# Kernel tuning notes

Hardware: AMD Instinct MI355X
Metric: run time of the kernel (lower is better)

## Reference

```python
import jax, jax.numpy as jnp
import numpy as np

B, L, DIM, H = 2, 2048, 1024, 16
HD = DIM // H  # head dim = 64
MASK_SCALE = -10 * 6  # faithful to the original source: mask_expand *= -10 * 6


def setup_inputs() -> dict:
    key = jax.random.key(0)
    ks = jax.random.split(key, 8)
    s = 1.0 / np.sqrt(DIM)
    return {
        "x": jax.random.normal(ks[0], (B, L, DIM), jnp.float32),
        "attention_mask": jax.random.uniform(ks[1], (B, L, L), jnp.float32),
        "Wq": jax.random.normal(ks[2], (DIM, DIM), jnp.float32) * s,
        "bq": jnp.zeros((DIM,), jnp.float32),
        "Wk": jax.random.normal(ks[3], (DIM, DIM), jnp.float32) * s,
        "bk": jnp.zeros((DIM,), jnp.float32),
        "Wv": jax.random.normal(ks[4], (DIM, DIM), jnp.float32) * s,
        "bv": jnp.zeros((DIM,), jnp.float32),
    }


def _split_heads(t):
    # [B, L, DIM] -> [B, H, L, HD]
    return t.reshape(B, L, H, HD).transpose(0, 2, 1, 3)


def reference(x, attention_mask, Wq, bq, Wk, bk, Wv, bv):
    q = _split_heads(x @ Wq + bq)
    k = _split_heads(x @ Wk + bk)
    v = _split_heads(x @ Wv + bv)
    scale = float(HD) ** -0.5
    # full [B, H, L, L] score matrix, as in the original
    scores = jnp.einsum("bhqd,bhkd->bhqk", q, k) * scale
    scores = scores + attention_mask[:, None, :, :] * MASK_SCALE
    probs = jax.nn.softmax(scores, axis=-1)
    ctx = jnp.einsum("bhqk,bhkd->bhqd", probs, v)
    # merge heads back: [B, L, DIM]
    return ctx.transpose(0, 2, 1, 3).reshape(B, L, DIM)
```

## Files before the change

kernel.cpp:

```cpp
#include <hip/hip_runtime.h>

#define LL 2048
#define NHEADS 16
#define HDIM 64
#define QSCALE 0.18033688011112042f
#define MASKC1 -86.56170245333780f

typedef __attribute__((ext_vector_type(8))) __bf16 bf16x8;
typedef __attribute__((ext_vector_type(4))) float f32x4;
typedef __attribute__((ext_vector_type(4))) unsigned int u32x4;

__device__ __forceinline__ unsigned short f2bf(float f) {
  unsigned int u = __builtin_bit_cast(unsigned int, f);
  u += 0x7fffu + ((u >> 16) & 1u);
  return (unsigned short)(u >> 16);
}

__device__ __forceinline__ bf16x8 ld_frag(const unsigned short* p) {
  return *reinterpret_cast<const bf16x8*>(p);
}

__device__ __forceinline__ float bflo(unsigned int u) {
  return __builtin_bit_cast(float, u << 16);
}
__device__ __forceinline__ float bfhi(unsigned int u) {
  return __builtin_bit_cast(float, u & 0xffff0000u);
}
__device__ __forceinline__ unsigned int pack2(float hi, float lo) {
  return __builtin_amdgcn_perm(__builtin_bit_cast(unsigned int, hi),
                               __builtin_bit_cast(unsigned int, lo), 0x07060302u);
}

__device__ __forceinline__ void async_cp16(const unsigned short* g, unsigned short* l) {
  __builtin_amdgcn_global_load_lds(
      (const __attribute__((address_space(1))) unsigned int*)(unsigned long long)(g),
      (__attribute__((address_space(3))) unsigned int*)(unsigned int)(unsigned long long)(l),
      16, 0, 0);
}

__global__ __launch_bounds__(256) void cvt_x_kernel(const float* __restrict__ x,
                                                    unsigned short* __restrict__ xb) {
  int i = (blockIdx.x * 256 + threadIdx.x) * 4;
  float4 v = *reinterpret_cast<const float4*>(x + i);
  ushort4 o;
  o.x = f2bf(v.x); o.y = f2bf(v.y); o.z = f2bf(v.z); o.w = f2bf(v.w);
  *reinterpret_cast<ushort4*>(xb + i) = o;
}

__global__ __launch_bounds__(256) void transpose_w_kernel(const float* __restrict__ Wq,
                                                          const float* __restrict__ Wk,
                                                          const float* __restrict__ Wv,
                                                          unsigned short* __restrict__ WtAll) {
  int z = blockIdx.z;
  const float* W = (z == 0) ? Wq : (z == 1) ? Wk : Wv;
  unsigned short* dst = WtAll + (size_t)z * 1024 * 1024;
  int n0 = blockIdx.x * 64, k0 = blockIdx.y * 64;
  __shared__ float t[64][65];
  int tx = threadIdx.x & 63, ty = threadIdx.x >> 6;
#pragma unroll
  for (int p = 0; p < 16; ++p) {
    int kr = p * 4 + ty;
    t[kr][tx] = W[(size_t)(k0 + kr) * 1024 + n0 + tx];
  }
  __syncthreads();
#pragma unroll
  for (int p = 0; p < 16; ++p) {
    int nr = p * 4 + ty;
    dst[(size_t)(n0 + nr) * 1024 + k0 + tx] = f2bf(t[tx][nr]);
  }
}

__global__ __launch_bounds__(256) void lem_prep_kernel(const float* __restrict__ mask,
                                                       unsigned short* __restrict__ lem) {
  const int qb = blockIdx.x, kt = blockIdx.y, b = blockIdx.z;
  const int tid = threadIdx.x;
  __shared__ unsigned short lds[128 * 72];
  {
    const int r0 = tid >> 4;
    const int c0 = (tid & 15) * 4;
#pragma unroll
    for (int p = 0; p < 8; ++p) {
      int row = p * 16 + r0;
      float4 v = *reinterpret_cast<const float4*>(
          mask + ((size_t)b * LL + qb * 128 + row) * LL + kt * 64 + c0);
      ushort4 o;
      o.x = f2bf(v.x * MASKC1); o.y = f2bf(v.y * MASKC1);
      o.z = f2bf(v.z * MASKC1); o.w = f2bf(v.w * MASKC1);
      *reinterpret_cast<ushort4*>(&lds[row * 72 + c0]) = o;
    }
  }
  __syncthreads();
  const int w = tid >> 6, lane = tid & 63, g = lane >> 4, cc = lane & 15;
  unsigned int ow[16];
#pragma unroll
  for (int mt = 0; mt < 2; ++mt) {
    const int q = w * 32 + mt * 16 + cc;
#pragma unroll
    for (int nt = 0; nt < 4; ++nt) {
      uint2 v = *reinterpret_cast<const uint2*>(&lds[q * 72 + nt * 16 + g * 4]);
      ow[mt * 8 + nt * 2]     = v.x;
      ow[mt * 8 + nt * 2 + 1] = v.y;
    }
  }
  uint4* dst = reinterpret_cast<uint4*>(
      lem + ((((size_t)b * 16 + qb) * 32 + kt) * 256 + tid) * 32);
#pragma unroll
  for (int j = 0; j < 4; ++j)
    dst[j] = make_uint4(ow[4 * j], ow[4 * j + 1], ow[4 * j + 2], ow[4 * j + 3]);
}

__global__ __launch_bounds__(256) void qkv_gemm_kernel(
    const unsigned short* __restrict__ xb, const unsigned short* __restrict__ WtAll,
    const float* __restrict__ bq, const float* __restrict__ bk, const float* __restrict__ bv,
    unsigned short* __restrict__ qkv) {
  const int z = blockIdx.z;
  const unsigned short* Wt = WtAll + (size_t)z * 1024 * 1024;
  const float* bias = (z == 0) ? bq : (z == 1) ? bk : bv;
  unsigned short* outb = qkv + (size_t)z * 4194304;

  __shared__ __align__(16) unsigned short smem[16384];
  unsigned short* As = smem;
  unsigned short* Bs = smem + 8192;

  const int tid = threadIdx.x;
  const int w = tid >> 6, lane = tid & 63, g = lane >> 4, cc = lane & 15;
  const int wm = w >> 1, wn = w & 1;
  const int m0 = blockIdx.y * 128, n0 = blockIdx.x * 128;
  const int srow = lane >> 3;
  const int gc = ((lane & 7) - srow) & 7;
  const unsigned short* ga = xb + (size_t)(m0 + w * 32 + srow) * 1024 + gc * 8;
  const unsigned short* gb = Wt + (size_t)(n0 + w * 32 + srow) * 1024 + gc * 8;
  unsigned short* la = As + w * 2048;
  unsigned short* lb = Bs + w * 2048;

  f32x4 acc[4][4];
#pragma unroll
  for (int i = 0; i < 4; ++i)
#pragma unroll
    for (int j = 0; j < 4; ++j) acc[i][j] = (f32x4)0.0f;

  for (int kk = 0; kk < 1024; kk += 64) {
    __syncthreads();
#pragma unroll
    for (int i = 0; i < 4; ++i) {
      async_cp16(ga + i * 8192 + kk, la + i * 512);
      async_cp16(gb + i * 8192 + kk, lb + i * 512);
    }
    __syncthreads();
    bf16x8 af[4][2], bfr[4][2];
#pragma unroll
    for (int mt = 0; mt < 4; ++mt)
#pragma unroll
      for (int ks = 0; ks < 2; ++ks)
        af[mt][ks] = ld_frag(&As[(wm * 64 + mt * 16 + cc) * 64 + ((4 * ks + g + cc) & 7) * 8]);
#pragma unroll
    for (int nt = 0; nt < 4; ++nt)
#pragma unroll
      for (int ks = 0; ks < 2; ++ks)
        bfr[nt][ks] = ld_frag(&Bs[(wn * 64 + nt * 16 + cc) * 64 + ((4 * ks + g + cc) & 7) * 8]);
#pragma unroll
    for (int mt = 0; mt < 4; ++mt)
#pragma unroll
      for (int nt = 0; nt < 4; ++nt)
#pragma unroll
        for (int ks = 0; ks < 2; ++ks)
          acc[mt][nt] = __builtin_amdgcn_mfma_f32_16x16x32_bf16(af[mt][ks], bfr[nt][ks],
                                                                acc[mt][nt], 0, 0, 0);
  }

  if (z != 2) {
    const float sc = (z == 0) ? QSCALE : 1.0f;
#pragma unroll
    for (int nt = 0; nt < 4; ++nt) {
      int n = n0 + wn * 64 + nt * 16 + cc;
      float bval = bias[n];
      int h = n >> 6, d = n & 63;
#pragma unroll
      for (int mt = 0; mt < 4; ++mt) {
#pragma unroll
        for (int r = 0; r < 4; ++r) {
          int m = m0 + wm * 64 + mt * 16 + g * 4 + r;
          int b = m >> 11, l = m & 2047;
          outb[(((size_t)(b * NHEADS + h) * LL) + l) * HDIM + d] =
              f2bf((acc[mt][nt][r] + bval) * sc);
        }
      }
    }
  } else {
    __syncthreads();
#pragma unroll
    for (int nt = 0; nt < 4; ++nt) {
      int nr = wn * 64 + nt * 16 + cc;
      float bval = bias[n0 + nr];
#pragma unroll
      for (int mt = 0; mt < 4; ++mt)
#pragma unroll
        for (int r = 0; r < 4; ++r)
          smem[nr * 128 + wm * 64 + (mt >> 1) * 32 + g * 8 + (mt & 1) * 4 + r] =
              f2bf(acc[mt][nt][r] + bval);
    }
    __syncthreads();
    int row = tid >> 1, half = tid & 1;
    int n = n0 + row, hh = n >> 6, dd = n & 63;
    int bb = m0 >> 11, l0 = (m0 & 2047) + half * 64;
    unsigned short* dst = outb + ((size_t)(bb * NHEADS + hh) * HDIM + dd) * LL + l0;
#pragma unroll
    for (int i = 0; i < 8; ++i)
      *reinterpret_cast<uint4*>(dst + i * 8) =
          *reinterpret_cast<const uint4*>(&smem[row * 128 + half * 64 + i * 8]);
  }
}

__global__ __launch_bounds__(256, 2) void flash_kernel(
    const unsigned short* __restrict__ Qb, const unsigned short* __restrict__ Kb,
    const unsigned short* __restrict__ Vt, const unsigned short* __restrict__ Lem,
    float* __restrict__ out) {
  const int id = blockIdx.y * 16 + blockIdx.x;
  const int nid = (id & 7) * 64 + (id >> 3);
  const int qb = nid & 15, bh = nid >> 4;
  const int b = bh >> 4, h = bh & 15;
  const int q0 = qb * 128;
  const int tid = threadIdx.x, w = tid >> 6, lane = tid & 63, g = lane >> 4, cc = lane & 15;
  const size_t bhoff = (size_t)bh * LL * HDIM;

  __shared__ __align__(16) unsigned short Ks[2][64 * 64];
  __shared__ __align__(16) unsigned short Vs[2][64 * 64];

  bf16x8 aq[2][2];
#pragma unroll
  for (int mt = 0; mt < 2; ++mt)
#pragma unroll
    for (int ks = 0; ks < 2; ++ks)
      aq[mt][ks] = *reinterpret_cast<const bf16x8*>(
          Qb + bhoff + (size_t)(q0 + w * 32 + mt * 16 + cc) * HDIM + ks * 32 + g * 8);

  const int srow = lane >> 3;
  const int gcs = ((lane & 7) - srow) & 7;
  const unsigned short* kg0 = Kb + bhoff + (size_t)(w * 8 + srow) * HDIM + gcs * 8;
  const unsigned short* kg1 = Kb + bhoff + (size_t)(32 + w * 8 + srow) * HDIM + gcs * 8;
  const unsigned short* vg0 = Vt + bhoff + (size_t)(w * 8 + srow) * LL + gcs * 8;
  const unsigned short* vg1 = Vt + bhoff + (size_t)(32 + w * 8 + srow) * LL + gcs * 8;

  const uint4* lemp = reinterpret_cast<const uint4*>(
      Lem + (((size_t)b * 16 + qb) * 32 * 256 + tid) * 32);

  const u32x4 onesu = {0x3F803F80u, 0x3F803F80u, 0x3F803F80u, 0x3F803F80u};
  const bf16x8 bones = __builtin_bit_cast(bf16x8, onesu);

  f32x4 liacc[2];
  f32x4 oacc[2][4];
#pragma unroll
  for (int mt = 0; mt < 2; ++mt) {
    liacc[mt] = (f32x4)0.0f;
#pragma unroll
    for (int nt = 0; nt < 4; ++nt) oacc[mt][nt] = (f32x4)0.0f;
  }

  async_cp16(kg0, Ks[0] + w * 512);
  async_cp16(kg1, Ks[0] + (w + 4) * 512);
  async_cp16(vg0, Vs[0] + w * 512);
  async_cp16(vg1, Vs[0] + (w + 4) * 512);
  uint4 e0 = lemp[0], e1 = lemp[1], e2 = lemp[2], e3 = lemp[3];
  lemp += 1024;

  for (int kt = 0; kt < 32; ++kt) {
    const int buf = kt & 1;
    __syncthreads();
    uint4 f0 = e0, f1 = e1, f2 = e2, f3 = e3;
    if (kt + 1 < 32) {
      const int nb = buf ^ 1;
      async_cp16(kg0 + (size_t)(kt + 1) * 64 * HDIM, Ks[nb] + w * 512);
      async_cp16(kg1 + (size_t)(kt + 1) * 64 * HDIM, Ks[nb] + (w + 4) * 512);
      async_cp16(vg0 + (kt + 1) * 64, Vs[nb] + w * 512);
      async_cp16(vg1 + (kt + 1) * 64, Vs[nb] + (w + 4) * 512);
      f0 = lemp[0]; f1 = lemp[1]; f2 = lemp[2]; f3 = lemp[3];
      lemp += 1024;
    }

    bf16x8 bk_[4][2];
#pragma unroll
    for (int nt = 0; nt < 4; ++nt)
#pragma unroll
      for (int ks = 0; ks < 2; ++ks)
        bk_[nt][ks] =
            ld_frag(&Ks[buf][(nt * 16 + cc) * 64 + ((4 * ks + g + cc) & 7) * 8]);
    bf16x8 bv[4][2];
#pragma unroll
    for (int nt = 0; nt < 4; ++nt)
#pragma unroll
      for (int ks = 0; ks < 2; ++ks)
        bv[nt][ks] =
            ld_frag(&Vs[buf][(nt * 16 + cc) * 64 + ((4 * ks + g + cc) & 7) * 8]);

    bf16x8 ap[2][2];
#pragma unroll
    for (int mt = 0; mt < 2; ++mt) {
      f32x4 sacc[4];
      const uint4 ea = (mt == 0) ? e0 : e2;
      const uint4 eb = (mt == 0) ? e1 : e3;
      sacc[0][0] = bflo(ea.x); sacc[0][1] = bfhi(ea.x);
      sacc[0][2] = bflo(ea.y); sacc[0][3] = bfhi(ea.y);
      sacc[1][0] = bflo(ea.z); sacc[1][1] = bfhi(ea.z);
      sacc[1][2] = bflo(ea.w); sacc[1][3] = bfhi(ea.w);
      sacc[2][0] = bflo(eb.x); sacc[2][1] = bfhi(eb.x);
      sacc[2][2] = bflo(eb.y); sacc[2][3] = bfhi(eb.y);
      sacc[3][0] = bflo(eb.z); sacc[3][1] = bfhi(eb.z);
      sacc[3][2] = bflo(eb.w); sacc[3][3] = bfhi(eb.w);
#pragma unroll
      for (int nt = 0; nt < 4; ++nt)
#pragma unroll
        for (int ks = 0; ks < 2; ++ks)
          sacc[nt] = __builtin_amdgcn_mfma_f32_16x16x32_bf16(bk_[nt][ks], aq[mt][ks],
                                                             sacc[nt], 0, 0, 0);
      float p[4][4];
#pragma unroll
      for (int nt = 0; nt < 4; ++nt)
#pragma unroll
        for (int r = 0; r < 4; ++r) p[nt][r] = __builtin_amdgcn_exp2f(sacc[nt][r]);
      unsigned int wd[8];
#pragma unroll
      for (int ks = 0; ks < 2; ++ks) {
        wd[ks * 4 + 0] = pack2(p[2 * ks][1],     p[2 * ks][0]);
        wd[ks * 4 + 1] = pack2(p[2 * ks][3],     p[2 * ks][2]);
        wd[ks * 4 + 2] = pack2(p[2 * ks + 1][1], p[2 * ks + 1][0]);
        wd[ks * 4 + 3] = pack2(p[2 * ks + 1][3], p[2 * ks + 1][2]);
        u32x4 uv = {wd[ks * 4], wd[ks * 4 + 1], wd[ks * 4 + 2], wd[ks * 4 + 3]};
        ap[mt][ks] = __builtin_bit_cast(bf16x8, uv);
      }
    }

#pragma unroll
    for (int mt = 0; mt < 2; ++mt) {
#pragma unroll
      for (int nt = 0; nt < 4; ++nt)
#pragma unroll
        for (int ks = 0; ks < 2; ++ks)
          oacc[mt][nt] = __builtin_amdgcn_mfma_f32_16x16x32_bf16(ap[mt][ks], bv[nt][ks],
                                                                 oacc[mt][nt], 0, 0, 0);
#pragma unroll
      for (int ks = 0; ks < 2; ++ks)
        liacc[mt] = __builtin_amdgcn_mfma_f32_16x16x32_bf16(ap[mt][ks], bones,
                                                            liacc[mt], 0, 0, 0);
    }

    e0 = f0; e1 = f1; e2 = f2; e3 = f3;
  }

#pragma unroll
  for (int mt = 0; mt < 2; ++mt) {
#pragma unroll
    for (int r = 0; r < 4; ++r) {
      float inv = 1.0f / liacc[mt][r];
      int qrow = q0 + w * 32 + mt * 16 + g * 4 + r;
#pragma unroll
      for (int nt = 0; nt < 4; ++nt)
        out[((size_t)b * LL + qrow) * 1024 + h * 64 + nt * 16 + cc] = oacc[mt][nt][r] * inv;
    }
  }
}

extern "C" void kernel_launch(void* const* d_in, const int* in_sizes, int n_in,
                              void* d_out, int out_size, void* d_ws, size_t ws_size,
                              hipStream_t stream) {
  const float* x    = (const float*)d_in[0];
  const float* mask = (const float*)d_in[1];
  const float* Wq   = (const float*)d_in[2];
  const float* bq   = (const float*)d_in[3];
  const float* Wk   = (const float*)d_in[4];
  const float* bk   = (const float*)d_in[5];
  const float* Wv   = (const float*)d_in[6];
  const float* bv   = (const float*)d_in[7];
  float* out = (float*)d_out;
  (void)in_sizes; (void)n_in; (void)out_size; (void)ws_size;

  char* ws = (char*)d_ws;
  unsigned short* qkv = (unsigned short*)(ws);
  unsigned short* xb  = (unsigned short*)(ws + (24u << 20));
  unsigned short* Wt  = (unsigned short*)(ws + (32u << 20));
  unsigned short* lem = (unsigned short*)(ws + (24u << 20));

  cvt_x_kernel<<<dim3(4096), dim3(256), 0, stream>>>(x, xb);
  transpose_w_kernel<<<dim3(16, 16, 3), dim3(256), 0, stream>>>(Wq, Wk, Wv, Wt);
  qkv_gemm_kernel<<<dim3(8, 32, 3), dim3(256), 0, stream>>>(xb, Wt, bq, bk, bv, qkv);
  lem_prep_kernel<<<dim3(16, 32, 2), dim3(256), 0, stream>>>(mask, lem);
  flash_kernel<<<dim3(16, 32), dim3(256), 0, stream>>>(qkv, qkv + 4194304, qkv + 8388608,
                                                       lem, out);
}
```

Baseline: 205.0 us.

## Triple-buffer K/V tiles with two-deep prefetch and manual vmcnt waits

```diff
diff --git a/kernel.cpp b/kernel.cpp
--- a/kernel.cpp
+++ b/kernel.cpp
@@ -36,6 +36,17 @@
       (const __attribute__((address_space(1))) unsigned int*)(unsigned long long)(g),
       (__attribute__((address_space(3))) unsigned int*)(unsigned int)(unsigned long long)(l),
       16, 0, 0);
+}
+
+__device__ __forceinline__ void lem_load(const unsigned short* p, uint4& a, uint4& b,
+                                         uint4& c, uint4& d) {
+  asm volatile("global_load_dwordx4 %0, %4, off\n\t"
+               "global_load_dwordx4 %1, %4, off offset:16\n\t"
+               "global_load_dwordx4 %2, %4, off offset:32\n\t"
+               "global_load_dwordx4 %3, %4, off offset:48"
+               : "=&v"(a), "=&v"(b), "=&v"(c), "=&v"(d)
+               : "v"(p)
+               : "memory");
 }
 
 __global__ __launch_bounds__(256) void cvt_x_kernel(const float* __restrict__ x,
@@ -223,8 +234,8 @@
   const int tid = threadIdx.x, w = tid >> 6, lane = tid & 63, g = lane >> 4, cc = lane & 15;
   const size_t bhoff = (size_t)bh * LL * HDIM;
 
-  __shared__ __align__(16) unsigned short Ks[2][64 * 64];
-  __shared__ __align__(16) unsigned short Vs[2][64 * 64];
+  __shared__ __align__(16) unsigned short Ks[3][64 * 64];
+  __shared__ __align__(16) unsigned short Vs[3][64 * 64];
 
   bf16x8 aq[2][2];
 #pragma unroll
@@ -241,11 +252,12 @@
   const unsigned short* vg0 = Vt + bhoff + (size_t)(w * 8 + srow) * LL + gcs * 8;
   const unsigned short* vg1 = Vt + bhoff + (size_t)(32 + w * 8 + srow) * LL + gcs * 8;
 
-  const uint4* lemp = reinterpret_cast<const uint4*>(
-      Lem + (((size_t)b * 16 + qb) * 32 * 256 + tid) * 32);
+  const unsigned short* lemq = Lem + (((size_t)b * 16 + qb) * 32 * 256 + tid) * 32;
 
   const u32x4 onesu = {0x3F803F80u, 0x3F803F80u, 0x3F803F80u, 0x3F803F80u};
   const bf16x8 bones = __builtin_bit_cast(bf16x8, onesu);
+
+  uint4 l00, l01, l02, l03, l10, l11, l12, l13, l20, l21, l22, l23;
 
   f32x4 liacc[2];
   f32x4 oacc[2][4];
@@ -260,91 +272,96 @@
   async_cp16(kg1, Ks[0] + (w + 4) * 512);
   async_cp16(vg0, Vs[0] + w * 512);
   async_cp16(vg1, Vs[0] + (w + 4) * 512);
-  uint4 e0 = lemp[0], e1 = lemp[1], e2 = lemp[2], e3 = lemp[3];
-  lemp += 1024;
-
-  for (int kt = 0; kt < 32; ++kt) {
-    const int buf = kt & 1;
-    __syncthreads();
-    uint4 f0 = e0, f1 = e1, f2 = e2, f3 = e3;
-    if (kt + 1 < 32) {
-      const int nb = buf ^ 1;
-      async_cp16(kg0 + (size_t)(kt + 1) * 64 * HDIM, Ks[nb] + w * 512);
-      async_cp16(kg1 + (size_t)(kt + 1) * 64 * HDIM, Ks[nb] + (w + 4) * 512);
-      async_cp16(vg0 + (kt + 1) * 64, Vs[nb] + w * 512);
-      async_cp16(vg1 + (kt + 1) * 64, Vs[nb] + (w + 4) * 512);
-      f0 = lemp[0]; f1 = lemp[1]; f2 = lemp[2]; f3 = lemp[3];
-      lemp += 1024;
-    }
-
-    bf16x8 bk_[4][2];
-#pragma unroll
-    for (int nt = 0; nt < 4; ++nt)
-#pragma unroll
-      for (int ks = 0; ks < 2; ++ks)
-        bk_[nt][ks] =
-            ld_frag(&Ks[buf][(nt * 16 + cc) * 64 + ((4 * ks + g + cc) & 7) * 8]);
-    bf16x8 bv[4][2];
-#pragma unroll
-    for (int nt = 0; nt < 4; ++nt)
-#pragma unroll
-      for (int ks = 0; ks < 2; ++ks)
-        bv[nt][ks] =
-            ld_frag(&Vs[buf][(nt * 16 + cc) * 64 + ((4 * ks + g + cc) & 7) * 8]);
-
-    bf16x8 ap[2][2];
-#pragma unroll
-    for (int mt = 0; mt < 2; ++mt) {
-      f32x4 sacc[4];
-      const uint4 ea = (mt == 0) ? e0 : e2;
-      const uint4 eb = (mt == 0) ? e1 : e3;
-      sacc[0][0] = bflo(ea.x); sacc[0][1] = bfhi(ea.x);
-      sacc[0][2] = bflo(ea.y); sacc[0][3] = bfhi(ea.y);
-      sacc[1][0] = bflo(ea.z); sacc[1][1] = bfhi(ea.z);
-      sacc[1][2] = bflo(ea.w); sacc[1][3] = bfhi(ea.w);
-      sacc[2][0] = bflo(eb.x); sacc[2][1] = bfhi(eb.x);
-      sacc[2][2] = bflo(eb.y); sacc[2][3] = bfhi(eb.y);
-      sacc[3][0] = bflo(eb.z); sacc[3][1] = bfhi(eb.z);
-      sacc[3][2] = bflo(eb.w); sacc[3][3] = bfhi(eb.w);
-#pragma unroll
-      for (int nt = 0; nt < 4; ++nt)
-#pragma unroll
-        for (int ks = 0; ks < 2; ++ks)
-          sacc[nt] = __builtin_amdgcn_mfma_f32_16x16x32_bf16(bk_[nt][ks], aq[mt][ks],
-                                                             sacc[nt], 0, 0, 0);
-      float p[4][4];
-#pragma unroll
-      for (int nt = 0; nt < 4; ++nt)
-#pragma unroll
-        for (int r = 0; r < 4; ++r) p[nt][r] = __builtin_amdgcn_exp2f(sacc[nt][r]);
-      unsigned int wd[8];
-#pragma unroll
-      for (int ks = 0; ks < 2; ++ks) {
-        wd[ks * 4 + 0] = pack2(p[2 * ks][1],     p[2 * ks][0]);
-        wd[ks * 4 + 1] = pack2(p[2 * ks][3],     p[2 * ks][2]);
-        wd[ks * 4 + 2] = pack2(p[2 * ks + 1][1], p[2 * ks + 1][0]);
-        wd[ks * 4 + 3] = pack2(p[2 * ks + 1][3], p[2 * ks + 1][2]);
-        u32x4 uv = {wd[ks * 4], wd[ks * 4 + 1], wd[ks * 4 + 2], wd[ks * 4 + 3]};
-        ap[mt][ks] = __builtin_bit_cast(bf16x8, uv);
-      }
-    }
-
-#pragma unroll
-    for (int mt = 0; mt < 2; ++mt) {
-#pragma unroll
-      for (int nt = 0; nt < 4; ++nt)
-#pragma unroll
-        for (int ks = 0; ks < 2; ++ks)
-          oacc[mt][nt] = __builtin_amdgcn_mfma_f32_16x16x32_bf16(ap[mt][ks], bv[nt][ks],
-                                                                 oacc[mt][nt], 0, 0, 0);
-#pragma unroll
-      for (int ks = 0; ks < 2; ++ks)
-        liacc[mt] = __builtin_amdgcn_mfma_f32_16x16x32_bf16(ap[mt][ks], bones,
-                                                            liacc[mt], 0, 0, 0);
-    }
-
-    e0 = f0; e1 = f1; e2 = f2; e3 = f3;
-  }
+  lem_load(lemq, l00, l01, l02, l03);
+  lemq += 8192;
+  async_cp16(kg0 + (size_t)64 * HDIM, Ks[1] + w * 512);
+  async_cp16(kg1 + (size_t)64 * HDIM, Ks[1] + (w + 4) * 512);
+  async_cp16(vg0 + 64, Vs[1] + w * 512);
+  async_cp16(vg1 + 64, Vs[1] + (w + 4) * 512);
+  lem_load(lemq, l10, l11, l12, l13);
+  lemq += 8192;
+
+#define FLASH_COMPUTE(BUF, LSA, LSB, LSC, LSD)                                         \
+  {                                                                                    \
+    bf16x8 bk_[4][2], bv[4][2];                                                        \
+    _Pragma("unroll") for (int nt = 0; nt < 4; ++nt)                                   \
+      _Pragma("unroll") for (int ks = 0; ks < 2; ++ks)                                 \
+        bk_[nt][ks] =                                                                  \
+            ld_frag(&Ks[BUF][(nt * 16 + cc) * 64 + ((4 * ks + g + cc) & 7) * 8]);      \
+    _Pragma("unroll") for (int nt = 0; nt < 4; ++nt)                                   \
+      _Pragma("unroll") for (int ks = 0; ks < 2; ++ks)                                 \
+        bv[nt][ks] =                                                                   \
+            ld_frag(&Vs[BUF][(nt * 16 + cc) * 64 + ((4 * ks + g + cc) & 7) * 8]);      \
+    bf16x8 ap[2][2];                                                                   \
+    _Pragma("unroll") for (int mt = 0; mt < 2; ++mt) {                                 \
+      f32x4 sacc[4];                                                                   \
+      const uint4 ea = (mt == 0) ? LSA : LSC;                                          \
+      const uint4 eb = (mt == 0) ? LSB : LSD;                                          \
+      sacc[0][0] = bflo(ea.x); sacc[0][1] = bfhi(ea.x);                                \
+      sacc[0][2] = bflo(ea.y); sacc[0][3] = bfhi(ea.y);                                \
+      sacc[1][0] = bflo(ea.z); sacc[1][1] = bfhi(ea.z);                                \
+      sacc[1][2] = bflo(ea.w); sacc[1][3] = bfhi(ea.w);                                \
+      sacc[2][0] = bflo(eb.x); sacc[2][1] = bfhi(eb.x);                                \
+      sacc[2][2] = bflo(eb.y); sacc[2][3] = bfhi(eb.y);                                \
+      sacc[3][0] = bflo(eb.z); sacc[3][1] = bfhi(eb.z);                                \
+      sacc[3][2] = bflo(eb.w); sacc[3][3] = bfhi(eb.w);                                \
+      _Pragma("unroll") for (int nt = 0; nt < 4; ++nt)                                 \
+        _Pragma("unroll") for (int ks = 0; ks < 2; ++ks)                               \
+          sacc[nt] = __builtin_amdgcn_mfma_f32_16x16x32_bf16(bk_[nt][ks], aq[mt][ks],  \
+                                                             sacc[nt], 0, 0, 0);       \
+      float p[4][4];                                                                   \
+      _Pragma("unroll") for (int nt = 0; nt < 4; ++nt)                                 \
+        _Pragma("unroll") for (int r = 0; r < 4; ++r)                                  \
+          p[nt][r] = __builtin_amdgcn_exp2f(sacc[nt][r]);                              \
+      unsigned int wd[8];                                                              \
+      _Pragma("unroll") for (int ks = 0; ks < 2; ++ks) {                               \
+        wd[ks * 4 + 0] = pack2(p[2 * ks][1],     p[2 * ks][0]);                        \
+        wd[ks * 4 + 1] = pack2(p[2 * ks][3],     p[2 * ks][2]);                        \
+        wd[ks * 4 + 2] = pack2(p[2 * ks + 1][1], p[2 * ks + 1][0]);                    \
+        wd[ks * 4 + 3] = pack2(p[2 * ks + 1][3], p[2 * ks + 1][2]);                    \
+        u32x4 uv = {wd[ks * 4], wd[ks * 4 + 1], wd[ks * 4 + 2], wd[ks * 4 + 3]};       \
+        ap[mt][ks] = __builtin_bit_cast(bf16x8, uv);                                   \
+      }                                                                                \
+    }                                                                                  \
+    _Pragma("unroll") for (int mt = 0; mt < 2; ++mt) {                                 \
+      _Pragma("unroll") for (int nt = 0; nt < 4; ++nt)                                 \
+        _Pragma("unroll") for (int ks = 0; ks < 2; ++ks)                               \
+          oacc[mt][nt] = __builtin_amdgcn_mfma_f32_16x16x32_bf16(ap[mt][ks], bv[nt][ks],\
+                                                                 oacc[mt][nt], 0, 0, 0);\
+      _Pragma("unroll") for (int ks = 0; ks < 2; ++ks)                                 \
+        liacc[mt] = __builtin_amdgcn_mfma_f32_16x16x32_bf16(ap[mt][ks], bones,         \
+                                                            liacc[mt], 0, 0, 0);       \
+    }                                                                                  \
+  }
+
+#define FITER(KT, CBUF, SBUF, VMC, ISSUE, UA, UB, UC, UD, LA, LB, LC, LD)              \
+  {                                                                                    \
+    asm volatile("s_waitcnt vmcnt(" VMC ")" ::: "memory");                             \
+    __builtin_amdgcn_sched_barrier(0);                                                 \
+    asm volatile("s_barrier" ::: "memory");                                            \
+    __builtin_amdgcn_sched_barrier(0);                                                 \
+    if (ISSUE) {                                                                       \
+      const size_t ko = (size_t)((KT) + 2) * 64;                                       \
+      async_cp16(kg0 + ko * HDIM, Ks[SBUF] + w * 512);                                 \
+      async_cp16(kg1 + ko * HDIM, Ks[SBUF] + (w + 4) * 512);                           \
+      async_cp16(vg0 + ko, Vs[SBUF] + w * 512);                                        \
+      async_cp16(vg1 + ko, Vs[SBUF] + (w + 4) * 512);                                  \
+      lem_load(lemq, LA, LB, LC, LD);                                                  \
+      lemq += 8192;                                                                    \
+    }                                                                                  \
+    FLASH_COMPUTE(CBUF, UA, UB, UC, UD);                                               \
+  }
+
+  for (int kt = 0; kt < 30; kt += 3) {
+    FITER(kt + 0, 0, 2, "8", true,  l00, l01, l02, l03, l20, l21, l22, l23)
+    FITER(kt + 1, 1, 0, "8", true,  l10, l11, l12, l13, l00, l01, l02, l03)
+    FITER(kt + 2, 2, 1, "8", true,  l20, l21, l22, l23, l10, l11, l12, l13)
+  }
+  FITER(30, 0, 0, "8", false, l00, l01, l02, l03, l00, l01, l02, l03)
+  FITER(31, 1, 0, "0", false, l10, l11, l12, l13, l10, l11, l12, l13)
+
+#undef FITER
+#undef FLASH_COMPUTE
 
 #pragma unroll
   for (int mt = 0; mt < 2; ++mt) {
```

Result: no change. 201.2 us (-1.8%).
